# Performance work log

Measured on AMD Instinct MI355X. Metric: run time of the kernel, lower is better.

Reference implementation:

```python
import jax, jax.numpy as jnp
import numpy as np

HEAD_DIM = 128
N_HEADS = 32
N_KV_HEADS = 8
EPS = 1e-6
ROPE_THETA = 1e6
NEG_INF = -1e9


def _rms_norm(x, w):
    # per-head RMSNorm over last dim (head_dim), fp32 math like Qwen3RMSNorm
    xf = x.astype(jnp.float32)
    var = jnp.mean(xf * xf, axis=-1, keepdims=True)
    return (w * (xf * jax.lax.rsqrt(var + EPS))).astype(x.dtype)


def _rope_cos_sin(position_ids, dtype):
    # default rope: inv_freq = theta^(-2i/d), emb = cat(freqs, freqs)
    inv_freq = 1.0 / (ROPE_THETA ** (jnp.arange(0, HEAD_DIM, 2, dtype=jnp.float32) / HEAD_DIM))
    freqs = position_ids.astype(jnp.float32)[:, :, None] * inv_freq[None, None, :]  # [B,S,hd/2]
    emb = jnp.concatenate([freqs, freqs], axis=-1)  # [B,S,hd]
    return jnp.cos(emb).astype(dtype), jnp.sin(emb).astype(dtype)


def _rotate_half(x):
    x1, x2 = jnp.split(x, 2, axis=-1)
    return jnp.concatenate([-x2, x1], axis=-1)


def setup_inputs() -> dict:
    key = jax.random.key(0)
    ks = jax.random.split(key, 6)
    B, S, H = 1, 2048, 4096
    return {
        "hidden_states": jax.random.normal(ks[0], (B, S, H), jnp.float32),
        "position_ids": jnp.broadcast_to(jnp.arange(S, dtype=jnp.int32)[None, :], (B, S)),
        "Wq": jax.random.normal(ks[1], (N_HEADS * HEAD_DIM, H), jnp.float32) * 0.02,
        "Wk": jax.random.normal(ks[2], (N_KV_HEADS * HEAD_DIM, H), jnp.float32) * 0.02,
        "Wv": jax.random.normal(ks[3], (N_KV_HEADS * HEAD_DIM, H), jnp.float32) * 0.02,
        "Wo": jax.random.normal(ks[4], (H, N_HEADS * HEAD_DIM), jnp.float32) * 0.02,
        "q_norm_w": jnp.ones((HEAD_DIM,), jnp.float32),
        "k_norm_w": jnp.ones((HEAD_DIM,), jnp.float32),
    }


def reference(hidden_states, position_ids, Wq, Wk, Wv, Wo, q_norm_w, k_norm_w):
    B, S, H = hidden_states.shape
    scaling = HEAD_DIM ** -0.5
    n_rep = N_HEADS // N_KV_HEADS

    # projections (torch Linear: y = x @ W.T), reshape to [B, heads, S, hd]
    q = jnp.einsum('bsh,dh->bsd', hidden_states, Wq).reshape(B, S, N_HEADS, HEAD_DIM)
    k = jnp.einsum('bsh,dh->bsd', hidden_states, Wk).reshape(B, S, N_KV_HEADS, HEAD_DIM)
    v = jnp.einsum('bsh,dh->bsd', hidden_states, Wv).reshape(B, S, N_KV_HEADS, HEAD_DIM)

    q = _rms_norm(q, q_norm_w).transpose(0, 2, 1, 3)  # [B,nH,S,hd]
    k = _rms_norm(k, k_norm_w).transpose(0, 2, 1, 3)  # [B,nKV,S,hd]
    v = v.transpose(0, 2, 1, 3)

    cos, sin = _rope_cos_sin(position_ids, hidden_states.dtype)
    cos = cos[:, None, :, :]  # unsqueeze head dim
    sin = sin[:, None, :, :]
    q = q * cos + _rotate_half(q) * sin
    k = k * cos + _rotate_half(k) * sin

    # GQA repeat_kv
    k = jnp.repeat(k, n_rep, axis=1)
    v = jnp.repeat(v, n_rep, axis=1)

    scores = jnp.einsum('bhqd,bhkd->bhqk', q, k) * scaling
    causal = jnp.where(
        jnp.arange(S)[:, None] >= jnp.arange(S)[None, :], 0.0, NEG_INF
    ).astype(scores.dtype)
    scores = scores + causal[None, None, :, :]
    attn = jax.nn.softmax(scores.astype(jnp.float32), axis=-1).astype(q.dtype)

    out = jnp.einsum('bhqk,bhkd->bhqd', attn, v)
    out = out.transpose(0, 2, 1, 3).reshape(B, S, N_HEADS * HEAD_DIM)
    return jnp.einsum('bsd,hd->bsh', out, Wo)
```

## Files before the change

### kernel.cpp

```cpp
#include <hip/hip_runtime.h>
#include <hip/hip_bf16.h>

typedef unsigned short u16;
typedef __bf16 bf16x8 __attribute__((ext_vector_type(8)));
typedef u16 u16x4 __attribute__((ext_vector_type(4)));
typedef u16 u16x8 __attribute__((ext_vector_type(8)));
typedef float f32x4 __attribute__((ext_vector_type(4)));

#define S_LEN  2048
#define HID    4096
#define NHEADS 32
#define NKV    8
#define HD     128
#define QDIM   (NHEADS*HD)
#define KVDIM  (NKV*HD)
#define NT     (S_LEN/64)

__device__ __forceinline__ u16 f2bf(float f) {
  unsigned u = __float_as_uint(f);
  u += 0x7fff + ((u >> 16) & 1);
  return (u16)(u >> 16);
}
__device__ __forceinline__ void lds_load16(const u16* g, u16* l) {
  __builtin_amdgcn_global_load_lds(
      (__attribute__((address_space(1))) void*)(g),
      (__attribute__((address_space(3))) void*)(l), 16, 0, 0);
}

__global__ __launch_bounds__(256) void f2b4(
    const float* __restrict__ s0, u16* __restrict__ d0, long n0,
    const float* __restrict__ s1, u16* __restrict__ d1, long n1,
    const float* __restrict__ s2, u16* __restrict__ d2, long n2,
    const float* __restrict__ s3, u16* __restrict__ d3, long n3)
{
  const float* s; u16* d; long n; int b0, nb;
  const int b = blockIdx.x;
  if (b < 1024)      { s=s0; d=d0; n=n0; b0=0;    nb=1024; }
  else if (b < 3072) { s=s1; d=d1; n=n1; b0=1024; nb=2048; }
  else if (b < 3584) { s=s2; d=d2; n=n2; b0=3072; nb=512;  }
  else               { s=s3; d=d3; n=n3; b0=3584; nb=512;  }
  long i = (long)(b - b0)*256 + threadIdx.x;
  const long stride = (long)nb*256;
  for (; i < n; i += stride) {
    f32x4 a = ((const f32x4*)s)[i*2];
    f32x4 c = ((const f32x4*)s)[i*2 + 1];
    u16x8 o;
    #pragma unroll
    for (int j = 0; j < 4; ++j) { o[j] = f2bf(a[j]); o[4+j] = f2bf(c[j]); }
    ((u16x8*)d)[i] = o;
  }
}

__global__ __launch_bounds__(256) void f2b(
    const float* __restrict__ in, u16* __restrict__ out, long n8)
{
  long i = (long)blockIdx.x * blockDim.x + threadIdx.x;
  const long stride = (long)gridDim.x * blockDim.x;
  for (; i < n8; i += stride) {
    f32x4 a = ((const f32x4*)in)[i*2];
    f32x4 b = ((const f32x4*)in)[i*2 + 1];
    u16x8 o;
    #pragma unroll
    for (int j = 0; j < 4; ++j) { o[j] = f2bf(a[j]); o[4+j] = f2bf(b[j]); }
    ((u16x8*)out)[i] = o;
  }
}

__global__ __launch_bounds__(512, 2) void gemmQ(
    const u16* __restrict__ A, const u16* __restrict__ B,
    u16* __restrict__ Cq, u16* __restrict__ Ck, u16* __restrict__ Cv,
    int K)
{
  __shared__ u16 lds[57344];
  const int tid  = threadIdx.x;
  const int lane = tid & 63;
  const int w    = tid >> 6;
  const int wr   = w >> 2, wc = w & 3;
  const int l16  = lane & 15, lhi = lane >> 4;
  const long arow0 = (long)blockIdx.y * 256;
  const long brow0 = (long)blockIdx.x * 192;
  const int ntiles = K >> 6;

  const int cu = ((lane & 7) ^ (lane >> 3)) * 8;
  const int wl = w*8 + (lane >> 3);
  const u16* Ag[4];
  #pragma unroll
  for (int r = 0; r < 4; ++r)
    Ag[r] = A + (arow0 + r*64 + wl)*(long)K + cu;
  const u16* Bg[3];
  #pragma unroll
  for (int r = 0; r < 2; ++r) {
    const int rp = r*64 + wl;
    Bg[r] = B + (brow0 + (rp >> 5)*48 + (rp & 31))*(long)K + cu;
  }
  Bg[2] = B + (brow0 + (wl >> 4)*48 + 32 + (wl & 15))*(long)K + cu;

  auto stageA = [&](int s, int kt) {
    u16* d = lds + ((kt & 1) << 14) + w*512;
    lds_load16(Ag[s]   + (long)kt*64, d + s*4096);
    lds_load16(Ag[s+2] + (long)kt*64, d + (s+2)*4096);
  };
  auto stageB0 = [&](int kt) {
    u16* d = lds + 32768 + (kt & 1)*12288 + w*512;
    lds_load16(Bg[0] + (long)kt*64, d);
    lds_load16(Bg[1] + (long)kt*64, d + 4096);
  };
  auto stageB1 = [&](int kt) {
    u16* d = lds + 32768 + (kt & 1)*12288 + w*512;
    lds_load16(Bg[2] + (long)kt*64, d + 8192);
  };

  const int xr = (l16 & 7) << 3;
  int offA[4][2], offB[2][2], offB2[2];
  #pragma unroll
  for (int m2 = 0; m2 < 4; ++m2)
    #pragma unroll
    for (int ks = 0; ks < 2; ++ks)
      offA[m2][ks] = (wr*128 + m2*16 + l16)*64 + ((ks*32 + lhi*8) ^ xr);
  #pragma unroll
  for (int n2 = 0; n2 < 2; ++n2)
    #pragma unroll
    for (int ks = 0; ks < 2; ++ks)
      offB[n2][ks] = (wc*32 + n2*16 + l16)*64 + ((ks*32 + lhi*8) ^ xr);
  #pragma unroll
  for (int ks = 0; ks < 2; ++ks)
    offB2[ks] = 8192 + (wc*16 + l16)*64 + ((ks*32 + lhi*8) ^ xr);

  f32x4 acc[8][3] = {};

  stageA(0, 0); stageB0(0); stageB1(0); stageA(1, 0);
  stageA(0, 1); stageB0(1); stageB1(1);
  asm volatile("s_waitcnt vmcnt(5)" ::: "memory");
  __builtin_amdgcn_s_barrier();

  #pragma unroll 2
  for (int t = 0; t < ntiles; ++t) {
    const int Ab = (t & 1) << 14;
    const int Bb = 32768 + (t & 1)*12288;
    bf16x8 af[4][2], af2[4][2], bf[2][2], bf2[2];

    #pragma unroll
    for (int m2 = 0; m2 < 4; ++m2)
      #pragma unroll
      for (int ks = 0; ks < 2; ++ks)
        af[m2][ks] = *(const bf16x8*)(lds + Ab + offA[m2][ks]);
    #pragma unroll
    for (int n2 = 0; n2 < 2; ++n2)
      #pragma unroll
      for (int ks = 0; ks < 2; ++ks)
        bf[n2][ks] = *(const bf16x8*)(lds + Bb + offB[n2][ks]);
    if (t + 1 < ntiles) stageA(1, t + 1);
    __builtin_amdgcn_s_barrier();
    asm volatile("s_waitcnt lgkmcnt(0)" ::: "memory");
    __builtin_amdgcn_s_setprio(1);
    #pragma unroll
    for (int m2 = 0; m2 < 4; ++m2)
      #pragma unroll
      for (int n2 = 0; n2 < 2; ++n2)
        #pragma unroll
        for (int ks = 0; ks < 2; ++ks)
          acc[m2][n2] = __builtin_amdgcn_mfma_f32_16x16x32_bf16(
              af[m2][ks], bf[n2][ks], acc[m2][n2], 0, 0, 0);
    __builtin_amdgcn_s_setprio(0);
    __builtin_amdgcn_s_barrier();

    #pragma unroll
    for (int ks = 0; ks < 2; ++ks)
      bf2[ks] = *(const bf16x8*)(lds + Bb + offB2[ks]);
    if (t + 2 < ntiles) stageA(0, t + 2);
    __builtin_amdgcn_s_barrier();
    asm volatile("s_waitcnt lgkmcnt(0)" ::: "memory");
    __builtin_amdgcn_s_setprio(1);
    #pragma unroll
    for (int m2 = 0; m2 < 4; ++m2)
      #pragma unroll
      for (int ks = 0; ks < 2; ++ks)
        acc[m2][2] = __builtin_amdgcn_mfma_f32_16x16x32_bf16(
            af[m2][ks], bf2[ks], acc[m2][2], 0, 0, 0);
    __builtin_amdgcn_s_setprio(0);
    __builtin_amdgcn_s_barrier();

    #pragma unroll
    for (int m2 = 0; m2 < 4; ++m2)
      #pragma unroll
      for (int ks = 0; ks < 2; ++ks)
        af2[m2][ks] = *(const bf16x8*)(lds + Ab + 4096 + offA[m2][ks]);
    if (t + 2 < ntiles) stageB0(t + 2);
    __builtin_amdgcn_s_barrier();
    asm volatile("s_waitcnt lgkmcnt(0)" ::: "memory");
    __builtin_amdgcn_s_setprio(1);
    #pragma unroll
    for (int m2 = 0; m2 < 4; ++m2)
      #pragma unroll
      for (int ks = 0; ks < 2; ++ks)
        acc[4+m2][2] = __builtin_amdgcn_mfma_f32_16x16x32_bf16(
            af2[m2][ks], bf2[ks], acc[4+m2][2], 0, 0, 0);
    __builtin_amdgcn_s_setprio(0);
    __builtin_amdgcn_s_barrier();

    if (t + 2 < ntiles) stageB1(t + 2);
    __builtin_amdgcn_s_barrier();
    __builtin_amdgcn_s_setprio(1);
    #pragma unroll
    for (int m2 = 0; m2 < 4; ++m2)
      #pragma unroll
      for (int n2 = 0; n2 < 2; ++n2)
        #pragma unroll
        for (int ks = 0; ks < 2; ++ks)
          acc[4+m2][n2] = __builtin_amdgcn_mfma_f32_16x16x32_bf16(
              af2[m2][ks], bf[n2][ks], acc[4+m2][n2], 0, 0, 0);
    __builtin_amdgcn_s_setprio(0);
    if (t + 2 < ntiles) { asm volatile("s_waitcnt vmcnt(5)" ::: "memory"); }
    else                { asm volatile("s_waitcnt vmcnt(0)" ::: "memory"); }
    __builtin_amdgcn_s_barrier();
  }

  #pragma unroll
  for (int m = 0; m < 8; ++m) {
    const long row = arow0 + wr*128 + (m >> 2)*64 + (m & 3)*16 + lhi*4;
    #pragma unroll
    for (int n = 0; n < 3; ++n) {
      const long col = brow0 + wc*48 + n*16 + l16;
      if (col < QDIM) {
        #pragma unroll
        for (int r = 0; r < 4; ++r)
          Cq[(row + r)*QDIM + col] = f2bf(acc[m][n][r]);
      } else if (col < QDIM + KVDIM) {
        #pragma unroll
        for (int r = 0; r < 4; ++r)
          Ck[(row + r)*KVDIM + (col - QDIM)] = f2bf(acc[m][n][r]);
      } else {
        u16x4 o;
        #pragma unroll
        for (int r = 0; r < 4; ++r) o[r] = f2bf(acc[m][n][r]);
        *(u16x4*)(Cv + (col - QDIM - KVDIM)*(long)S_LEN + row) = o;
      }
    }
  }
}

__global__ __launch_bounds__(512, 2) void gemmF(
    const u16* __restrict__ A, const u16* __restrict__ B,
    float* __restrict__ C, int M, int N, int K)
{
  __shared__ u16 lds[49152];
  const int tid  = threadIdx.x;
  const int lane = tid & 63;
  const int w    = tid >> 6;
  const int wr   = w >> 2, wc = w & 3;
  const int l16  = lane & 15, lhi = lane >> 4;
  const long arow0 = (long)blockIdx.y * 128;
  const long brow0 = (long)blockIdx.x * 256;
  const int ntiles = K >> 6;

  const int cu = ((lane & 7) ^ (lane >> 3)) * 8;
  const int rA  = (w >> 2)*64 + (w & 3)*8;
  const int rB1c = 128 + (w >> 2)*64 + (w & 3)*8;
  const u16* srcA  = A + (arow0 + rA   + (lane >> 3))*(long)K + cu;
  const u16* srcB0 = B + (brow0 + rA   + (lane >> 3))*(long)K + cu;
  const u16* srcB1 = B + (brow0 + rB1c + (lane >> 3))*(long)K + cu;
  u16* const dA  = lds + rA*64;
  u16* const dB0 = lds + 16384 + rA*64;
  u16* const dB1 = lds + 16384 + rB1c*64;

  auto stageA = [&](int s, int kt) {
    lds_load16(srcA + (long)(s*32)*K + kt*64,
               dA + ((kt & 1) << 13) + s*2048);
  };
  auto stageB = [&](int s, int kt) {
    const long so = (long)(s*32)*K + kt*64;
    const int  d  = ((kt & 1) << 14) + s*2048;
    lds_load16(srcB0 + so, dB0 + d);
    lds_load16(srcB1 + so, dB1 + d);
  };

  const int xr = (l16 & 7) << 3;
  int offA[2][2], offB[2][2];
  #pragma unroll
  for (int m = 0; m < 2; ++m)
    #pragma unroll
    for (int ks = 0; ks < 2; ++ks)
      offA[m][ks] = (wr*64 + m*16 + l16)*64 + ((ks*32 + lhi*8) ^ xr);
  #pragma unroll
  for (int n = 0; n < 2; ++n)
    #pragma unroll
    for (int ks = 0; ks < 2; ++ks)
      offB[n][ks] = (wc*64 + n*16 + l16)*64 + ((ks*32 + lhi*8) ^ xr);

  f32x4 acc[4][4] = {};

  stageA(0, 0); stageA(1, 0); stageB(0, 0); stageB(1, 0);
  if (ntiles > 1) { stageA(0, 1); stageB(0, 1); stageB(1, 1); }
  asm volatile("s_waitcnt vmcnt(5)" ::: "memory");
  __builtin_amdgcn_s_barrier();

  #pragma unroll 2
  for (int t = 0; t < ntiles; ++t) {
    const int Ab = (t & 1) << 13;
    const int Bb = 16384 + ((t & 1) << 14);
    bf16x8 af[2][2], bf[2][2], af2[2][2], bf2[2][2];

    #pragma unroll
    for (int m = 0; m < 2; ++m)
      #pragma unroll
      for (int ks = 0; ks < 2; ++ks)
        af[m][ks] = *(const bf16x8*)(lds + Ab + offA[m][ks]);
    #pragma unroll
    for (int n = 0; n < 2; ++n)
      #pragma unroll
      for (int ks = 0; ks < 2; ++ks)
        bf[n][ks] = *(const bf16x8*)(lds + Bb + offB[n][ks]);
    if (t + 1 < ntiles) stageA(1, t + 1);
    __builtin_amdgcn_s_barrier();
    asm volatile("s_waitcnt lgkmcnt(0)" ::: "memory");
    __builtin_amdgcn_s_setprio(1);
    #pragma unroll
    for (int m = 0; m < 2; ++m)
      #pragma unroll
      for (int n = 0; n < 2; ++n)
        #pragma unroll
        for (int ks = 0; ks < 2; ++ks)
          acc[m][n] = __builtin_amdgcn_mfma_f32_16x16x32_bf16(
              af[m][ks], bf[n][ks], acc[m][n], 0, 0, 0);
    __builtin_amdgcn_s_setprio(0);
    __builtin_amdgcn_s_barrier();

    #pragma unroll
    for (int n = 0; n < 2; ++n)
      #pragma unroll
      for (int ks = 0; ks < 2; ++ks)
        bf2[n][ks] = *(const bf16x8*)(lds + Bb + 2048 + offB[n][ks]);
    if (t + 2 < ntiles) stageA(0, t + 2);
    __builtin_amdgcn_s_barrier();
    asm volatile("s_waitcnt lgkmcnt(0)" ::: "memory");
    __builtin_amdgcn_s_setprio(1);
    #pragma unroll
    for (int m = 0; m < 2; ++m)
      #pragma unroll
      for (int n = 0; n < 2; ++n)
        #pragma unroll
        for (int ks = 0; ks < 2; ++ks)
          acc[m][2+n] = __builtin_amdgcn_mfma_f32_16x16x32_bf16(
              af[m][ks], bf2[n][ks], acc[m][2+n], 0, 0, 0);
    __builtin_amdgcn_s_setprio(0);
    __builtin_amdgcn_s_barrier();

    #pragma unroll
    for (int m = 0; m < 2; ++m)
      #pragma unroll
      for (int ks = 0; ks < 2; ++ks)
        af2[m][ks] = *(const bf16x8*)(lds + Ab + 2048 + offA[m][ks]);
    if (t + 2 < ntiles) stageB(0, t + 2);
    __builtin_amdgcn_s_barrier();
    asm volatile("s_waitcnt lgkmcnt(0)" ::: "memory");
    __builtin_amdgcn_s_setprio(1);
    #pragma unroll
    for (int m = 0; m < 2; ++m)
      #pragma unroll
      for (int n = 0; n < 2; ++n)
        #pragma unroll
        for (int ks = 0; ks < 2; ++ks)
          acc[2+m][2+n] = __builtin_amdgcn_mfma_f32_16x16x32_bf16(
              af2[m][ks], bf2[n][ks], acc[2+m][2+n], 0, 0, 0);
    __builtin_amdgcn_s_setprio(0);
    __builtin_amdgcn_s_barrier();

    if (t + 2 < ntiles) stageB(1, t + 2);
    __builtin_amdgcn_s_barrier();
    __builtin_amdgcn_s_setprio(1);
    #pragma unroll
    for (int m = 0; m < 2; ++m)
      #pragma unroll
      for (int n = 0; n < 2; ++n)
        #pragma unroll
        for (int ks = 0; ks < 2; ++ks)
          acc[2+m][n] = __builtin_amdgcn_mfma_f32_16x16x32_bf16(
              af2[m][ks], bf[n][ks], acc[2+m][n], 0, 0, 0);
    __builtin_amdgcn_s_setprio(0);
    if (t + 2 < ntiles) { asm volatile("s_waitcnt vmcnt(5)" ::: "memory"); }
    else                { asm volatile("s_waitcnt vmcnt(0)" ::: "memory"); }
    __builtin_amdgcn_s_barrier();
  }

  #pragma unroll
  for (int mi = 0; mi < 4; ++mi) {
    const long row = arow0 + wr*64 + (mi >> 1)*32 + (mi & 1)*16 + lhi*4;
    #pragma unroll
    for (int ni = 0; ni < 4; ++ni) {
      const long col = brow0 + wc*64 + (ni >> 1)*32 + (ni & 1)*16 + l16;
      #pragma unroll
      for (int r = 0; r < 4; ++r)
        C[(row + r)*N + col] = acc[mi][ni][r];
    }
  }
}

__global__ __launch_bounds__(256) void norm_rope2(
    u16* __restrict__ Qb, u16* __restrict__ Kb,
    const float* __restrict__ qw, const float* __restrict__ kw,
    const int* __restrict__ pos)
{
  const int row  = blockIdx.x * 4 + (threadIdx.x >> 6);
  const int lane = threadIdx.x & 63;
  u16* p; const float* nw; float sc; int s;
  if (row < S_LEN*NHEADS) {
    p = Qb + (long)row * HD; nw = qw; sc = 0.08838834764831845f; s = row >> 5;
  } else {
    const int r2 = row - S_LEN*NHEADS;
    p = Kb + (long)r2 * HD; nw = kw; sc = 1.0f; s = r2 >> 3;
  }

  float x1 = __uint_as_float(((unsigned)p[lane]) << 16);
  float x2 = __uint_as_float(((unsigned)p[lane + 64]) << 16);
  float ss = x1*x1 + x2*x2;
  #pragma unroll
  for (int m = 32; m >= 1; m >>= 1) ss += __shfl_xor(ss, m);
  const float inv = rsqrtf(ss * (1.0f/128.0f) + 1e-6f);
  x1 *= inv * nw[lane];
  x2 *= inv * nw[lane + 64];

  const float inv_freq = expf(-(float)lane * (13.815510557964274f / 64.0f));
  const float ang = (float)pos[s] * inv_freq;
  float sn, cs;
  sincosf(ang, &sn, &cs);
  p[lane]      = f2bf((x1*cs - x2*sn) * sc);
  p[lane + 64] = f2bf((x2*cs + x1*sn) * sc);
}

__global__ __launch_bounds__(256, 4) void attn(
    const u16* __restrict__ Q, const u16* __restrict__ K,
    const u16* __restrict__ VT, u16* __restrict__ O)
{
  __shared__ u16 Ks[64*128];
  __shared__ u16 Vt[128*64];
  __shared__ u16 Ps[4*16*64];

  const int tid  = threadIdx.x;
  const int lane = tid & 63;
  const int w    = tid >> 6;
  const int l16  = lane & 15, lhi = lane >> 4;

  const int x8  = blockIdx.x & 7;
  const int idx = blockIdx.x >> 3;
  const int cc  = idx & 31;
  const int jj  = idx >> 5;
  const int h   = x8*4 + jj;
  const int kh  = x8;
  const int T   = (jj & 1) ? cc : (NT - 1) - cc;
  const int qrow0 = T*64 + w*16;

  bf16x8 qf[4];
  #pragma unroll
  for (int ks = 0; ks < 4; ++ks)
    qf[ks] = *(const bf16x8*)(Q + (long)(qrow0 + l16)*QDIM + h*HD + ks*32 + lhi*8);

  float mr[4] = {-1e30f,-1e30f,-1e30f,-1e30f};
  float lr[4] = {0.f,0.f,0.f,0.f};
  f32x4 of[8] = {};
  u16* Pw = Ps + w*16*64;

  for (int t = 0; t <= T; ++t) {
    const int kv0 = t * 64;
    #pragma unroll
    for (int i = 0; i < 4; ++i) {
      const int r   = w*16 + i*4 + lhi;
      const int col = (l16*8) ^ ((r & 7) << 3);
      lds_load16(K + (long)(kv0 + r)*KVDIM + kh*HD + col,
                 Ks + (w*16 + i*4)*128);
    }
    #pragma unroll
    for (int i = 0; i < 4; ++i) {
      const int r   = w*32 + i*8 + (lane >> 3);
      const int col = ((lane & 7)*8) ^ ((r & 7) << 3);
      lds_load16(VT + (long)(kh*HD + r)*S_LEN + kv0 + col,
                 Vt + (w*32 + i*8)*64);
    }
    __syncthreads();

    f32x4 sa[4] = {};
    __builtin_amdgcn_s_setprio(1);
    #pragma unroll
    for (int n = 0; n < 4; ++n)
      #pragma unroll
      for (int ks = 0; ks < 4; ++ks) {
        bf16x8 kf = *(const bf16x8*)(
            Ks + (n*16 + l16)*128 + ((ks*32 + lhi*8) ^ ((l16 & 7) << 3)));
        sa[n] = __builtin_amdgcn_mfma_f32_16x16x32_bf16(qf[ks], kf, sa[n], 0, 0, 0);
      }
    __builtin_amdgcn_s_setprio(0);

    const bool diag = (t == T);
    float pm[4];
    #pragma unroll
    for (int r = 0; r < 4; ++r) {
      const int grow = qrow0 + lhi*4 + r;
      #pragma unroll
      for (int n = 0; n < 4; ++n) {
        float sv = sa[n][r];
        if (diag && (kv0 + n*16 + l16 > grow)) sv = -1e9f;
        sa[n][r] = sv;
      }
      float p01 = fmaxf(sa[0][r], sa[1][r]);
      float p23 = fmaxf(sa[2][r], sa[3][r]);
      float pmx = fmaxf(p01, p23);
      pmx = fmaxf(pmx, __shfl_xor(pmx, 1));
      pmx = fmaxf(pmx, __shfl_xor(pmx, 2));
      pmx = fmaxf(pmx, __shfl_xor(pmx, 4));
      pmx = fmaxf(pmx, __shfl_xor(pmx, 8));
      pm[r] = pmx;
    }
    bool need = (pm[0] > mr[0] + 8.f) | (pm[1] > mr[1] + 8.f) |
                (pm[2] > mr[2] + 8.f) | (pm[3] > mr[3] + 8.f);
    if (__any(need)) {
      #pragma unroll
      for (int r = 0; r < 4; ++r) {
        const float mnew  = fmaxf(mr[r], pm[r]);
        const float alpha = __expf(mr[r] - mnew);
        mr[r] = mnew;
        lr[r] *= alpha;
        #pragma unroll
        for (int c = 0; c < 8; ++c) of[c][r] *= alpha;
      }
    }
    #pragma unroll
    for (int r = 0; r < 4; ++r) {
      float rsum = 0.f;
      #pragma unroll
      for (int n = 0; n < 4; ++n) {
        float pv = __expf(sa[n][r] - mr[r]);
        sa[n][r] = pv;
        rsum += pv;
      }
      rsum += __shfl_xor(rsum, 1);
      rsum += __shfl_xor(rsum, 2);
      rsum += __shfl_xor(rsum, 4);
      rsum += __shfl_xor(rsum, 8);
      lr[r] += rsum;
    }

    #pragma unroll
    for (int r = 0; r < 4; ++r) {
      const int prow = lhi*4 + r;
      #pragma unroll
      for (int n = 0; n < 4; ++n)
        Pw[prow*64 + ((n*16 + l16) ^ ((prow & 7) << 3))] = f2bf(sa[n][r]);
    }
    __builtin_amdgcn_s_setprio(1);
    #pragma unroll
    for (int ks = 0; ks < 2; ++ks) {
      bf16x8 pf = *(const bf16x8*)(
          Pw + l16*64 + ((ks*32 + lhi*8) ^ ((l16 & 7) << 3)));
      #pragma unroll
      for (int c = 0; c < 8; ++c) {
        bf16x8 vf = *(const bf16x8*)(
            Vt + (c*16 + l16)*64 + ((ks*32 + lhi*8) ^ ((l16 & 7) << 3)));
        of[c] = __builtin_amdgcn_mfma_f32_16x16x32_bf16(pf, vf, of[c], 0, 0, 0);
      }
    }
    __builtin_amdgcn_s_setprio(0);
    __syncthreads();
  }

  #pragma unroll
  for (int r = 0; r < 4; ++r) {
    const float invl = 1.0f / lr[r];
    const long orow = (long)(qrow0 + lhi*4 + r) * QDIM + h*HD;
    #pragma unroll
    for (int c = 0; c < 8; ++c)
      O[orow + c*16 + l16] = f2bf(of[c][r] * invl);
  }
}

extern "C" void kernel_launch(void* const* d_in, const int* in_sizes, int n_in,
                              void* d_out, int out_size, void* d_ws, size_t ws_size,
                              hipStream_t stream) {
  (void)in_sizes; (void)n_in; (void)out_size; (void)ws_size;
  const float* hs  = (const float*)d_in[0];
  const int*   pos = (const int*)d_in[1];
  const float* Wq  = (const float*)d_in[2];
  const float* Wk  = (const float*)d_in[3];
  const float* Wv  = (const float*)d_in[4];
  const float* Wo  = (const float*)d_in[5];
  const float* qw  = (const float*)d_in[6];
  const float* kw  = (const float*)d_in[7];

  u16* hsB = (u16*)d_ws;
  u16* W1  = hsB + (long)S_LEN*HID;
  u16* WkB = W1  + (long)QDIM*HID;
  u16* WvB = WkB + (long)KVDIM*HID;
  u16* Kb  = WvB + (long)KVDIM*HID;
  u16* VT  = Kb  + (long)S_LEN*KVDIM;
  u16* AO  = VT  + (long)KVDIM*S_LEN;
  u16* Qb  = (u16*)d_out;

  f2b4<<<4096, 256, 0, stream>>>(hs, hsB, (long)S_LEN*HID/8,
                                 Wq, W1,  (long)QDIM*HID/8,
                                 Wk, WkB, (long)KVDIM*HID/8,
                                 Wv, WvB, (long)KVDIM*HID/8);

  gemmQ<<<dim3((QDIM+2*KVDIM)/192, S_LEN/256), 512, 0, stream>>>(
      hsB, W1, Qb, Kb, VT, HID);

  norm_rope2<<<(S_LEN*NHEADS + S_LEN*NKV)/4, 256, 0, stream>>>(
      Qb, Kb, qw, kw, pos);

  f2b<<<2048, 256, 0, stream>>>(Wo, W1, (long)HID*QDIM/8);

  attn<<<dim3(NT*NHEADS), 256, 0, stream>>>(Qb, Kb, VT, AO);

  gemmF<<<dim3(HID/256, S_LEN/128), 512, 0, stream>>>(
      AO, W1, (float*)d_out, S_LEN, HID, QDIM);
}
```

Baseline: 341.7 us.

## Prefetch attention K/V tiles into registers one iteration ahead

Replaces the direct global-to-LDS loads in the attention loop with register prefetch. The next K/V tile is read from global memory while the current tile's MFMAs run, then written to LDS at the top of the next iteration, with explicit waitcnt and barriers. The aim is to hide global load latency behind compute. It costs extra VGPRs for the staging registers, which may reduce occupancy. The GEMM kernels also take their K/N dimensions as template constants so the compiler can specialize them.

```diff
diff --git a/kernel.cpp b/kernel.cpp
--- a/kernel.cpp
+++ b/kernel.cpp
@@ -66,10 +66,10 @@
   }
 }
 
+template<int K>
 __global__ __launch_bounds__(512, 2) void gemmQ(
     const u16* __restrict__ A, const u16* __restrict__ B,
-    u16* __restrict__ Cq, u16* __restrict__ Ck, u16* __restrict__ Cv,
-    int K)
+    u16* __restrict__ Cq, u16* __restrict__ Ck, u16* __restrict__ Cv)
 {
   __shared__ u16 lds[57344];
   const int tid  = threadIdx.x;
@@ -239,9 +239,10 @@
   }
 }
 
+template<int N, int K>
 __global__ __launch_bounds__(512, 2) void gemmF(
     const u16* __restrict__ A, const u16* __restrict__ B,
-    float* __restrict__ C, int M, int N, int K)
+    float* __restrict__ C)
 {
   __shared__ u16 lds[49152];
   const int tid  = threadIdx.x;
@@ -454,28 +455,52 @@
   for (int ks = 0; ks < 4; ++ks)
     qf[ks] = *(const bf16x8*)(Q + (long)(qrow0 + l16)*QDIM + h*HD + ks*32 + lhi*8);
 
+  const u16* kbase[4]; int kld[4];
+  const u16* vbase[4]; int vld[4];
+  #pragma unroll
+  for (int i = 0; i < 4; ++i) {
+    const int r   = w*16 + i*4 + lhi;
+    const int col = (l16*8) ^ ((r & 7) << 3);
+    kbase[i] = K + (long)r*KVDIM + kh*HD + col;
+    kld[i]   = (w*16 + i*4)*128 + lane*8;
+  }
+  #pragma unroll
+  for (int i = 0; i < 4; ++i) {
+    const int r   = w*32 + i*8 + (lane >> 3);
+    const int col = ((lane & 7)*8) ^ ((r & 7) << 3);
+    vbase[i] = VT + (long)(kh*HD + r)*S_LEN + col;
+    vld[i]   = (w*32 + i*8)*64 + lane*8;
+  }
+
   float mr[4] = {-1e30f,-1e30f,-1e30f,-1e30f};
   float lr[4] = {0.f,0.f,0.f,0.f};
   f32x4 of[8] = {};
   u16* Pw = Ps + w*16*64;
 
+  u16x8 kreg[4], vreg[4];
+  #pragma unroll
+  for (int i = 0; i < 4; ++i) kreg[i] = *(const u16x8*)(kbase[i]);
+  #pragma unroll
+  for (int i = 0; i < 4; ++i) vreg[i] = *(const u16x8*)(vbase[i]);
+
   for (int t = 0; t <= T; ++t) {
+    #pragma unroll
+    for (int i = 0; i < 4; ++i) *(u16x8*)(Ks + kld[i]) = kreg[i];
+    #pragma unroll
+    for (int i = 0; i < 4; ++i) *(u16x8*)(Vt + vld[i]) = vreg[i];
+    asm volatile("s_waitcnt lgkmcnt(0)" ::: "memory");
+    __builtin_amdgcn_s_barrier();
+
+    if (t < T) {
+      const long ko = (long)(t + 1) * 64 * KVDIM;
+      const int  vo = (t + 1) * 64;
+      #pragma unroll
+      for (int i = 0; i < 4; ++i) kreg[i] = *(const u16x8*)(kbase[i] + ko);
+      #pragma unroll
+      for (int i = 0; i < 4; ++i) vreg[i] = *(const u16x8*)(vbase[i] + vo);
+    }
+
     const int kv0 = t * 64;
-    #pragma unroll
-    for (int i = 0; i < 4; ++i) {
-      const int r   = w*16 + i*4 + lhi;
-      const int col = (l16*8) ^ ((r & 7) << 3);
-      lds_load16(K + (long)(kv0 + r)*KVDIM + kh*HD + col,
-                 Ks + (w*16 + i*4)*128);
-    }
-    #pragma unroll
-    for (int i = 0; i < 4; ++i) {
-      const int r   = w*32 + i*8 + (lane >> 3);
-      const int col = ((lane & 7)*8) ^ ((r & 7) << 3);
-      lds_load16(VT + (long)(kh*HD + r)*S_LEN + kv0 + col,
-                 Vt + (w*32 + i*8)*64);
-    }
-    __syncthreads();
 
     f32x4 sa[4] = {};
     __builtin_amdgcn_s_setprio(1);
@@ -558,7 +583,8 @@
       }
     }
     __builtin_amdgcn_s_setprio(0);
-    __syncthreads();
+    asm volatile("s_waitcnt lgkmcnt(0)" ::: "memory");
+    __builtin_amdgcn_s_barrier();
   }
 
   #pragma unroll
@@ -598,8 +624,8 @@
                                  Wk, WkB, (long)KVDIM*HID/8,
                                  Wv, WvB, (long)KVDIM*HID/8);
 
-  gemmQ<<<dim3((QDIM+2*KVDIM)/192, S_LEN/256), 512, 0, stream>>>(
-      hsB, W1, Qb, Kb, VT, HID);
+  gemmQ<HID><<<dim3((QDIM+2*KVDIM)/192, S_LEN/256), 512, 0, stream>>>(
+      hsB, W1, Qb, Kb, VT);
 
   norm_rope2<<<(S_LEN*NHEADS + S_LEN*NKV)/4, 256, 0, stream>>>(
       Qb, Kb, qw, kw, pos);
@@ -608,6 +634,6 @@
 
   attn<<<dim3(NT*NHEADS), 256, 0, stream>>>(Qb, Kb, VT, AO);
 
-  gemmF<<<dim3(HID/256, S_LEN/128), 512, 0, stream>>>(
-      AO, W1, (float*)d_out, S_LEN, HID, QDIM);
-}
+  gemmF<HID, QDIM><<<dim3(HID/256, S_LEN/128), 512, 0, stream>>>(
+      AO, W1, (float*)d_out);
+}
```

Measured after the change: 495.2 us. +44.9%, slower.

## Shrink QKV GEMM tile to 128 rows and template K/N as compile-time constants

Applied to the files above, without the earlier changes.

The fused QKV projection GEMM drops from a 256x192 to a 128x192 output tile. That halves the A staging buffers and accumulators, and the launch bound is raised to 4 blocks per SM. The grid doubles along M, which gives more blocks for the CUs to balance. The pipeline schedule is reshuffled: A is staged in one step and the B loads are spread across phases, with wait counts adjusted. K and N become template parameters in both GEMMs, so loop counts and strides are compile-time constants. The smaller tile lowers arithmetic intensity and increases global traffic for B.

```diff
diff --git a/kernel.cpp b/kernel.cpp
--- a/kernel.cpp
+++ b/kernel.cpp
@@ -66,26 +66,26 @@
   }
 }
 
-__global__ __launch_bounds__(512, 2) void gemmQ(
+template<int K>
+__global__ __launch_bounds__(512, 4) void gemmQ(
     const u16* __restrict__ A, const u16* __restrict__ B,
-    u16* __restrict__ Cq, u16* __restrict__ Ck, u16* __restrict__ Cv,
-    int K)
+    u16* __restrict__ Cq, u16* __restrict__ Ck, u16* __restrict__ Cv)
 {
-  __shared__ u16 lds[57344];
+  __shared__ u16 lds[40960];
   const int tid  = threadIdx.x;
   const int lane = tid & 63;
   const int w    = tid >> 6;
   const int wr   = w >> 2, wc = w & 3;
   const int l16  = lane & 15, lhi = lane >> 4;
-  const long arow0 = (long)blockIdx.y * 256;
+  const long arow0 = (long)blockIdx.y * 128;
   const long brow0 = (long)blockIdx.x * 192;
   const int ntiles = K >> 6;
 
   const int cu = ((lane & 7) ^ (lane >> 3)) * 8;
   const int wl = w*8 + (lane >> 3);
-  const u16* Ag[4];
-  #pragma unroll
-  for (int r = 0; r < 4; ++r)
+  const u16* Ag[2];
+  #pragma unroll
+  for (int r = 0; r < 2; ++r)
     Ag[r] = A + (arow0 + r*64 + wl)*(long)K + cu;
   const u16* Bg[3];
   #pragma unroll
@@ -95,28 +95,28 @@
   }
   Bg[2] = B + (brow0 + (wl >> 4)*48 + 32 + (wl & 15))*(long)K + cu;
 
-  auto stageA = [&](int s, int kt) {
-    u16* d = lds + ((kt & 1) << 14) + w*512;
-    lds_load16(Ag[s]   + (long)kt*64, d + s*4096);
-    lds_load16(Ag[s+2] + (long)kt*64, d + (s+2)*4096);
+  auto stageA = [&](int kt) {
+    u16* d = lds + ((kt & 1) << 13) + w*512;
+    lds_load16(Ag[0] + (long)kt*64, d);
+    lds_load16(Ag[1] + (long)kt*64, d + 4096);
   };
   auto stageB0 = [&](int kt) {
-    u16* d = lds + 32768 + (kt & 1)*12288 + w*512;
+    u16* d = lds + 16384 + (kt & 1)*12288 + w*512;
     lds_load16(Bg[0] + (long)kt*64, d);
     lds_load16(Bg[1] + (long)kt*64, d + 4096);
   };
   auto stageB1 = [&](int kt) {
-    u16* d = lds + 32768 + (kt & 1)*12288 + w*512;
+    u16* d = lds + 16384 + (kt & 1)*12288 + w*512;
     lds_load16(Bg[2] + (long)kt*64, d + 8192);
   };
 
   const int xr = (l16 & 7) << 3;
-  int offA[4][2], offB[2][2], offB2[2];
-  #pragma unroll
-  for (int m2 = 0; m2 < 4; ++m2)
+  int offA[2][2], offB[2][2], offB2[2];
+  #pragma unroll
+  for (int m2 = 0; m2 < 2; ++m2)
     #pragma unroll
     for (int ks = 0; ks < 2; ++ks)
-      offA[m2][ks] = (wr*128 + m2*16 + l16)*64 + ((ks*32 + lhi*8) ^ xr);
+      offA[m2][ks] = (wr*64 + m2*16 + l16)*64 + ((ks*32 + lhi*8) ^ xr);
   #pragma unroll
   for (int n2 = 0; n2 < 2; ++n2)
     #pragma unroll
@@ -126,21 +126,21 @@
   for (int ks = 0; ks < 2; ++ks)
     offB2[ks] = 8192 + (wc*16 + l16)*64 + ((ks*32 + lhi*8) ^ xr);
 
-  f32x4 acc[8][3] = {};
-
-  stageA(0, 0); stageB0(0); stageB1(0); stageA(1, 0);
-  stageA(0, 1); stageB0(1); stageB1(1);
-  asm volatile("s_waitcnt vmcnt(5)" ::: "memory");
+  f32x4 acc[4][3] = {};
+
+  stageA(0); stageB0(0); stageB1(0);
+  stageB0(1); stageB1(1);
+  asm volatile("s_waitcnt vmcnt(3)" ::: "memory");
   __builtin_amdgcn_s_barrier();
 
   #pragma unroll 2
   for (int t = 0; t < ntiles; ++t) {
-    const int Ab = (t & 1) << 14;
-    const int Bb = 32768 + (t & 1)*12288;
-    bf16x8 af[4][2], af2[4][2], bf[2][2], bf2[2];
-
-    #pragma unroll
-    for (int m2 = 0; m2 < 4; ++m2)
+    const int Ab = (t & 1) << 13;
+    const int Bb = 16384 + (t & 1)*12288;
+    bf16x8 af[2][2], af2[2][2], bf[2][2], bf2[2];
+
+    #pragma unroll
+    for (int m2 = 0; m2 < 2; ++m2)
       #pragma unroll
       for (int ks = 0; ks < 2; ++ks)
         af[m2][ks] = *(const bf16x8*)(lds + Ab + offA[m2][ks]);
@@ -149,12 +149,12 @@
       #pragma unroll
       for (int ks = 0; ks < 2; ++ks)
         bf[n2][ks] = *(const bf16x8*)(lds + Bb + offB[n2][ks]);
-    if (t + 1 < ntiles) stageA(1, t + 1);
+    if (t + 1 < ntiles) stageA(t + 1);
     __builtin_amdgcn_s_barrier();
     asm volatile("s_waitcnt lgkmcnt(0)" ::: "memory");
     __builtin_amdgcn_s_setprio(1);
     #pragma unroll
-    for (int m2 = 0; m2 < 4; ++m2)
+    for (int m2 = 0; m2 < 2; ++m2)
       #pragma unroll
       for (int n2 = 0; n2 < 2; ++n2)
         #pragma unroll
@@ -167,12 +167,12 @@
     #pragma unroll
     for (int ks = 0; ks < 2; ++ks)
       bf2[ks] = *(const bf16x8*)(lds + Bb + offB2[ks]);
-    if (t + 2 < ntiles) stageA(0, t + 2);
+    if (t + 2 < ntiles) stageB0(t + 2);
     __builtin_amdgcn_s_barrier();
     asm volatile("s_waitcnt lgkmcnt(0)" ::: "memory");
     __builtin_amdgcn_s_setprio(1);
     #pragma unroll
-    for (int m2 = 0; m2 < 4; ++m2)
+    for (int m2 = 0; m2 < 2; ++m2)
       #pragma unroll
       for (int ks = 0; ks < 2; ++ks)
         acc[m2][2] = __builtin_amdgcn_mfma_f32_16x16x32_bf16(
@@ -181,43 +181,41 @@
     __builtin_amdgcn_s_barrier();
 
     #pragma unroll
-    for (int m2 = 0; m2 < 4; ++m2)
-      #pragma unroll
-      for (int ks = 0; ks < 2; ++ks)
-        af2[m2][ks] = *(const bf16x8*)(lds + Ab + 4096 + offA[m2][ks]);
-    if (t + 2 < ntiles) stageB0(t + 2);
+    for (int m2 = 0; m2 < 2; ++m2)
+      #pragma unroll
+      for (int ks = 0; ks < 2; ++ks)
+        af2[m2][ks] = *(const bf16x8*)(lds + Ab + 2048 + offA[m2][ks]);
+    if (t + 2 < ntiles) stageB1(t + 2);
     __builtin_amdgcn_s_barrier();
     asm volatile("s_waitcnt lgkmcnt(0)" ::: "memory");
     __builtin_amdgcn_s_setprio(1);
     #pragma unroll
-    for (int m2 = 0; m2 < 4; ++m2)
-      #pragma unroll
-      for (int ks = 0; ks < 2; ++ks)
-        acc[4+m2][2] = __builtin_amdgcn_mfma_f32_16x16x32_bf16(
-            af2[m2][ks], bf2[ks], acc[4+m2][2], 0, 0, 0);
-    __builtin_amdgcn_s_setprio(0);
-    __builtin_amdgcn_s_barrier();
-
-    if (t + 2 < ntiles) stageB1(t + 2);
-    __builtin_amdgcn_s_barrier();
-    __builtin_amdgcn_s_setprio(1);
-    #pragma unroll
-    for (int m2 = 0; m2 < 4; ++m2)
+    for (int m2 = 0; m2 < 2; ++m2)
+      #pragma unroll
+      for (int ks = 0; ks < 2; ++ks)
+        acc[2+m2][2] = __builtin_amdgcn_mfma_f32_16x16x32_bf16(
+            af2[m2][ks], bf2[ks], acc[2+m2][2], 0, 0, 0);
+    __builtin_amdgcn_s_setprio(0);
+    __builtin_amdgcn_s_barrier();
+
+    __builtin_amdgcn_s_setprio(1);
+    #pragma unroll
+    for (int m2 = 0; m2 < 2; ++m2)
       #pragma unroll
       for (int n2 = 0; n2 < 2; ++n2)
         #pragma unroll
         for (int ks = 0; ks < 2; ++ks)
-          acc[4+m2][n2] = __builtin_amdgcn_mfma_f32_16x16x32_bf16(
-              af2[m2][ks], bf[n2][ks], acc[4+m2][n2], 0, 0, 0);
-    __builtin_amdgcn_s_setprio(0);
-    if (t + 2 < ntiles) { asm volatile("s_waitcnt vmcnt(5)" ::: "memory"); }
+          acc[2+m2][n2] = __builtin_amdgcn_mfma_f32_16x16x32_bf16(
+              af2[m2][ks], bf[n2][ks], acc[2+m2][n2], 0, 0, 0);
+    __builtin_amdgcn_s_setprio(0);
+    if (t + 2 < ntiles) { asm volatile("s_waitcnt vmcnt(3)" ::: "memory"); }
     else                { asm volatile("s_waitcnt vmcnt(0)" ::: "memory"); }
     __builtin_amdgcn_s_barrier();
   }
 
   #pragma unroll
-  for (int m = 0; m < 8; ++m) {
-    const long row = arow0 + wr*128 + (m >> 2)*64 + (m & 3)*16 + lhi*4;
+  for (int m = 0; m < 4; ++m) {
+    const long row = arow0 + wr*64 + m*16 + lhi*4;
     #pragma unroll
     for (int n = 0; n < 3; ++n) {
       const long col = brow0 + wc*48 + n*16 + l16;
@@ -239,9 +237,10 @@
   }
 }
 
+template<int N, int K>
 __global__ __launch_bounds__(512, 2) void gemmF(
     const u16* __restrict__ A, const u16* __restrict__ B,
-    float* __restrict__ C, int M, int N, int K)
+    float* __restrict__ C)
 {
   __shared__ u16 lds[49152];
   const int tid  = threadIdx.x;
@@ -598,8 +597,8 @@
                                  Wk, WkB, (long)KVDIM*HID/8,
                                  Wv, WvB, (long)KVDIM*HID/8);
 
-  gemmQ<<<dim3((QDIM+2*KVDIM)/192, S_LEN/256), 512, 0, stream>>>(
-      hsB, W1, Qb, Kb, VT, HID);
+  gemmQ<HID><<<dim3((QDIM+2*KVDIM)/192, S_LEN/128), 512, 0, stream>>>(
+      hsB, W1, Qb, Kb, VT);
 
   norm_rope2<<<(S_LEN*NHEADS + S_LEN*NKV)/4, 256, 0, stream>>>(
       Qb, Kb, qw, kw, pos);
@@ -608,6 +607,6 @@
 
   attn<<<dim3(NT*NHEADS), 256, 0, stream>>>(Qb, Kb, VT, AO);
 
-  gemmF<<<dim3(HID/256, S_LEN/128), 512, 0, stream>>>(
-      AO, W1, (float*)d_out, S_LEN, HID, QDIM);
-}
+  gemmF<HID, QDIM><<<dim3(HID/256, S_LEN/128), 512, 0, stream>>>(
+      AO, W1, (float*)d_out);
+}
```

After: 330.8 us. 3.2% less time.
